# Performance work log

Measured on AMD Instinct MI355X. Metric: run time of the kernel, lower is better.

Reference implementation:

```python
import jax, jax.numpy as jnp
import numpy as np

B, N, H, E, D = 8, 2048, 1024, 8, 2048


def setup_inputs() -> dict:
    key = jax.random.key(0)
    k = jax.random.split(key, 5)
    x = jax.random.normal(k[0], (B, N, H), dtype=jnp.float32)
    Wr = jax.random.normal(k[1], (H, E), dtype=jnp.float32) * 0.02
    br = jnp.zeros((E,), dtype=jnp.float32)
    W1 = jax.random.normal(k[2], (E, H, D), dtype=jnp.float32) * 0.02
    b1 = jnp.zeros((E, D), dtype=jnp.float32)
    W2 = jax.random.normal(k[3], (E, D, H), dtype=jnp.float32) * 0.02
    b2 = jnp.zeros((E, H), dtype=jnp.float32)
    return {"x": x, "Wr": Wr, "br": br, "W1": W1, "b1": b1, "W2": W2, "b2": b2}


def reference(x, Wr, br, W1, b1, W2, b2):
    # x: [B,N,H]; router v1, top-1, eval mode (no expert dropout)
    Bx, Nx, Hx = x.shape
    Ex = Wr.shape[1]
    x_flat = x.reshape(Bx * Nx, Hx)                      # [T,H]
    logits = x_flat @ Wr + br                            # [T,E]
    probs = jax.nn.softmax(logits, axis=-1)              # [T,E]
    expert_idx = jnp.argmax(probs, axis=-1)              # [T]

    out_flat = jnp.zeros_like(x_flat)
    for e in range(Ex):  # small fixed loop over experts
        h = jax.nn.gelu(x_flat @ W1[e] + b1[e], approximate=False)  # exact erf GELU (torch default)
        eout = h @ W2[e] + b2[e]                         # [T,H]
        out_flat = jnp.where((expert_idx == e)[:, None], eout, out_flat)

    out = x + out_flat.reshape(Bx, Nx, Hx)               # residual

    p_i = probs.mean(axis=0)                             # [E]
    balance_loss = Ex * jnp.sum(p_i ** 2)
    EPS = 1e-8
    entropy = -jnp.sum(probs * jnp.log(probs + EPS), axis=-1)
    entropy_loss = entropy.mean()
    tokens_per_expert = jnp.bincount(expert_idx, length=Ex)
    return out, balance_loss, entropy_loss, tokens_per_expert
```

## Files before the change

### kernel.cpp

```cpp
#include <hip/hip_runtime.h>
#include <math.h>

#define TT 16384
#define HH 1024
#define DD 2048
#define EE 8
#define MAXTILES 160

typedef float f32x4 __attribute__((ext_vector_type(4)));
typedef __bf16 bf16x8 __attribute__((ext_vector_type(8)));

__device__ __forceinline__ unsigned short f2bf(float f) {
  union { float f; unsigned u; } v; v.f = f;
  unsigned r = v.u + 0x7FFFu + ((v.u >> 16) & 1u);
  return (unsigned short)(r >> 16);
}

__device__ __forceinline__ void gl2lds16(const unsigned short* g, unsigned short* l) {
  __builtin_amdgcn_global_load_lds(
      (const __attribute__((address_space(1))) void*)g,
      (__attribute__((address_space(3))) void*)l, 16, 0, 0);
}

__global__ void k_init(int* counts, float* probs_sum, float* ent_sum) {
  int t = threadIdx.x;
  if (t < EE) { counts[t] = 0; probs_sum[t] = 0.f; }
  if (t == 0) *ent_sum = 0.f;
}

__global__ __launch_bounds__(256) void k_transpose2(const float* __restrict__ W1s,
                                                    unsigned short* __restrict__ W1d,
                                                    const float* __restrict__ W2s,
                                                    unsigned short* __restrict__ W2d) {
  const int T1 = EE * (HH / 64) * (DD / 64);
  int bid = blockIdx.x;
  const float* src; unsigned short* dst; int R, C;
  if (bid < T1) { src = W1s; dst = W1d; R = HH; C = DD; }
  else          { bid -= T1; src = W2s; dst = W2d; R = DD; C = HH; }
  int tilesC = C >> 6, tilesR = R >> 6;
  int e = bid / (tilesR * tilesC);
  int rem = bid % (tilesR * tilesC);
  int tr = rem / tilesC, tc = rem % tilesC;
  const float* s = src + (size_t)e * R * C + (size_t)(tr * 64) * C + tc * 64;
  unsigned short* d = dst + (size_t)e * R * C + (size_t)(tc * 64) * R + tr * 64;

  __shared__ float t2[64][65];
  int t = threadIdx.x;
  int col = t & 63, rbase = t >> 6;
#pragma unroll
  for (int i = 0; i < 16; ++i) {
    int row = rbase + i * 4;
    t2[col][row] = s[(size_t)row * C + col];
  }
  __syncthreads();
#pragma unroll
  for (int i = 0; i < 4; ++i) {
    int p = t + i * 256;
    int rr = p >> 4, ch = (p & 15) << 2;
    ushort4 o;
    o.x = f2bf(t2[rr][ch + 0]);
    o.y = f2bf(t2[rr][ch + 1]);
    o.z = f2bf(t2[rr][ch + 2]);
    o.w = f2bf(t2[rr][ch + 3]);
    *(ushort4*)&d[(size_t)rr * R + ch] = o;
  }
}

__global__ __launch_bounds__(256) void k_router(const float* __restrict__ x,
                                                const float* __restrict__ Wr,
                                                const float* __restrict__ br,
                                                int* __restrict__ eidx,
                                                float* __restrict__ probs_sum,
                                                float* __restrict__ ent_sum,
                                                int* __restrict__ counts,
                                                unsigned short* __restrict__ xb) {
  __shared__ float s_p[EE];
  __shared__ int   s_c[EE];
  __shared__ float s_e;
  int tid = threadIdx.x;
  if (tid < EE) { s_p[tid] = 0.f; s_c[tid] = 0; }
  if (tid == 0) s_e = 0.f;
  __syncthreads();
  int lane = tid & 63, w = tid >> 6;
  for (int tt = 0; tt < 4; ++tt) {
    int token = blockIdx.x * 16 + w * 4 + tt;
    double acc[EE];
#pragma unroll
    for (int e = 0; e < EE; ++e) acc[e] = 0.0;
    const float* xr = x + (size_t)token * HH;
    unsigned short* xo = xb + (size_t)token * HH;
#pragma unroll
    for (int i = 0; i < 4; ++i) {
      int hh = i * 256 + lane * 4;
      f32x4 xf = *(const f32x4*)&xr[hh];
      ushort4 o;
      o.x = f2bf(xf[0]); o.y = f2bf(xf[1]); o.z = f2bf(xf[2]); o.w = f2bf(xf[3]);
      *(ushort4*)&xo[hh] = o;
#pragma unroll
      for (int k = 0; k < 4; ++k) {
        double xv = (double)xf[k];
        const float* wr = Wr + (size_t)(hh + k) * EE;
#pragma unroll
        for (int e = 0; e < EE; ++e) acc[e] += xv * (double)wr[e];
      }
    }
#pragma unroll
    for (int off = 32; off > 0; off >>= 1) {
#pragma unroll
      for (int e = 0; e < EE; ++e) acc[e] += __shfl_down(acc[e], off);
    }
    if (lane == 0) {
      double l[EE];
#pragma unroll
      for (int e = 0; e < EE; ++e) l[e] = acc[e] + (double)br[e];
      double m = l[0]; int am = 0;
#pragma unroll
      for (int e = 1; e < EE; ++e) { if (l[e] > m) { m = l[e]; am = e; } }
      float p[EE]; float s = 0.f;
#pragma unroll
      for (int e = 0; e < EE; ++e) { p[e] = __expf((float)(l[e] - m)); s += p[e]; }
      float inv = 1.0f / s; float ent = 0.f;
#pragma unroll
      for (int e = 0; e < EE; ++e) { p[e] *= inv; ent -= p[e] * __logf(p[e] + 1e-8f); }
      eidx[token] = am;
#pragma unroll
      for (int e = 0; e < EE; ++e) atomicAdd(&s_p[e], p[e]);
      atomicAdd(&s_e, ent);
      atomicAdd(&s_c[am], 1);
    }
  }
  __syncthreads();
  if (tid < EE) { atomicAdd(&probs_sum[tid], s_p[tid]); atomicAdd(&counts[tid], s_c[tid]); }
  if (tid == 0) atomicAdd(ent_sum, s_e);
}

__global__ __launch_bounds__(256) void k_scan(const int* counts, const float* probs_sum,
                       const float* ent_sum, int* offsets, int* cursor,
                       int* tileE, int* tileR0, int* tileEnd, int* nTiles,
                       float* out_scalars) {
  __shared__ int soff[EE + 1];
  __shared__ int tbase[EE + 1];
  int t = threadIdx.x;
  if (t == 0) {
    int off = 0, tb = 0;
    for (int e = 0; e < EE; ++e) {
      soff[e] = off; offsets[e] = off; cursor[e] = off;
      tbase[e] = tb;
      tb += (counts[e] + 127) >> 7;
      off += counts[e];
    }
    soff[EE] = off; offsets[EE] = off; tbase[EE] = tb;
    *nTiles = tb;
    float bal = 0.f;
    for (int e = 0; e < EE; ++e) { float pi = probs_sum[e] / (float)TT; bal += pi * pi; }
    out_scalars[0] = (float)EE * bal;
    out_scalars[1] = *ent_sum / (float)TT;
    for (int e = 0; e < EE; ++e) out_scalars[2 + e] = (float)counts[e];
  }
  __syncthreads();
  int nt = tbase[EE];
  for (int i = t; i < nt; i += 256) {
    int e = 0;
    while (tbase[e + 1] <= i) ++e;
    int j = i - tbase[e];
    tileE[i] = e; tileR0[i] = soff[e] + j * 128; tileEnd[i] = soff[e] + counts[e];
  }
}

__global__ __launch_bounds__(256) void k_perm(const int* __restrict__ eidx,
                                              int* cursor, int* __restrict__ perm) {
  int t = blockIdx.x * 256 + threadIdx.x;
  int lane = threadIdx.x & 63;
  int mye = eidx[t];
  int pos = 0;
#pragma unroll
  for (int e = 0; e < EE; ++e) {
    unsigned long long mask = __ballot(mye == e);
    if (mask == 0ull) continue;
    int leader = __ffsll(mask) - 1;
    int base = 0;
    if (lane == leader) base = atomicAdd(&cursor[e], __popcll(mask));
    base = __shfl(base, leader);
    if (mye == e) pos = base + (int)__popcll(mask & ((1ull << lane) - 1ull));
  }
  perm[pos] = t;
}


__global__ __launch_bounds__(256) void k_gemm1(const unsigned short* __restrict__ xb,
                                               const unsigned short* __restrict__ Wt1,
                                               const float* __restrict__ b1,
                                               const int* __restrict__ perm,
                                               const int* __restrict__ tileE,
                                               const int* __restrict__ tileR0,
                                               const int* __restrict__ tileEnd,
                                               const int* __restrict__ nTiles,
                                               unsigned short* __restrict__ hbuf) {
  int tile = blockIdx.y;
  if (tile >= *nTiles) return;
  int e = tileE[tile], r0 = tileR0[tile], rend = tileEnd[tile];
  int c0 = blockIdx.x * 128;
  __shared__ __align__(16) unsigned short As[128 * 32];
  __shared__ __align__(16) unsigned short Bs[128 * 32];
  int tid = threadIdx.x, lane = tid & 63, w = tid >> 6;
  int wr = w >> 1, wc = w & 1;
  int quad = lane >> 4, l16 = lane & 15;
  int srow = lane >> 2, seg = lane & 3;
  int ar0 = w * 32 + srow, ar1 = ar0 + 16;
  int g0 = r0 + ar0; if (g0 >= rend) g0 = rend - 1;
  int g1 = r0 + ar1; if (g1 >= rend) g1 = rend - 1;
  const unsigned short* aG0 = xb + (size_t)perm[g0] * HH + seg * 8;
  const unsigned short* aG1 = xb + (size_t)perm[g1] * HH + seg * 8;
  const unsigned short* bBase = Wt1 + (size_t)e * ((size_t)DD * HH);
  const unsigned short* bG0 = bBase + (size_t)(c0 + ar0) * HH + seg * 8;
  const unsigned short* bG1 = bBase + (size_t)(c0 + ar1) * HH + seg * 8;
  unsigned short* aL0 = &As[(w * 32 + 0) * 32];
  unsigned short* aL1 = &As[(w * 32 + 16) * 32];
  unsigned short* bL0 = &Bs[(w * 32 + 0) * 32];
  unsigned short* bL1 = &Bs[(w * 32 + 16) * 32];
  f32x4 acc[4][4] = {};
  for (int k0 = 0; k0 < HH; k0 += 32) {
    gl2lds16(aG0 + k0, aL0);
    gl2lds16(aG1 + k0, aL1);
    gl2lds16(bG0 + k0, bL0);
    gl2lds16(bG1 + k0, bL1);
    __syncthreads();
    bf16x8 a[4], b[4];
#pragma unroll
    for (int i = 0; i < 4; ++i)
      a[i] = *(const bf16x8*)&As[(wr * 64 + i * 16 + l16) * 32 + quad * 8];
#pragma unroll
    for (int j = 0; j < 4; ++j)
      b[j] = *(const bf16x8*)&Bs[(wc * 64 + j * 16 + l16) * 32 + quad * 8];
#pragma unroll
    for (int i = 0; i < 4; ++i)
#pragma unroll
      for (int j = 0; j < 4; ++j)
        acc[i][j] = __builtin_amdgcn_mfma_f32_16x16x32_bf16(a[i], b[j], acc[i][j], 0, 0, 0);
    __syncthreads();
  }
  float bias[4];
#pragma unroll
  for (int j = 0; j < 4; ++j) bias[j] = b1[e * DD + c0 + wc * 64 + j * 16 + l16];
#pragma unroll
  for (int i = 0; i < 4; ++i) {
#pragma unroll
    for (int r = 0; r < 4; ++r) {
      int gr = r0 + wr * 64 + i * 16 + quad * 4 + r;
      if (gr < rend) {
#pragma unroll
        for (int j = 0; j < 4; ++j) {
          int col = c0 + wc * 64 + j * 16 + l16;
          float v = acc[i][j][r] + bias[j];
          v = 0.5f * v * (1.0f + erff(v * 0.70710678118654752f));
          hbuf[(size_t)gr * DD + col] = f2bf(v);
        }
      }
    }
  }
}

__global__ __launch_bounds__(256) void k_gemm2(const unsigned short* __restrict__ hbuf,
                                               const unsigned short* __restrict__ Wt2,
                                               const float* __restrict__ b2,
                                               const float* __restrict__ x,
                                               const int* __restrict__ perm,
                                               const int* __restrict__ tileE,
                                               const int* __restrict__ tileR0,
                                               const int* __restrict__ tileEnd,
                                               const int* __restrict__ nTiles,
                                               float* __restrict__ outp) {
  int tile = blockIdx.y;
  if (tile >= *nTiles) return;
  int e = tileE[tile], r0 = tileR0[tile], rend = tileEnd[tile];
  int c0 = blockIdx.x * 128;
  __shared__ __align__(16) unsigned short As[128 * 32];
  __shared__ __align__(16) unsigned short Bs[128 * 32];
  int tid = threadIdx.x, lane = tid & 63, w = tid >> 6;
  int wr = w >> 1, wc = w & 1;
  int quad = lane >> 4, l16 = lane & 15;
  int srow = lane >> 2, seg = lane & 3;
  int ar0 = w * 32 + srow, ar1 = ar0 + 16;
  int g0 = r0 + ar0; if (g0 >= rend) g0 = rend - 1;
  int g1 = r0 + ar1; if (g1 >= rend) g1 = rend - 1;
  const unsigned short* aG0 = hbuf + (size_t)g0 * DD + seg * 8;
  const unsigned short* aG1 = hbuf + (size_t)g1 * DD + seg * 8;
  const unsigned short* bBase = Wt2 + (size_t)e * ((size_t)HH * DD);
  const unsigned short* bG0 = bBase + (size_t)(c0 + ar0) * DD + seg * 8;
  const unsigned short* bG1 = bBase + (size_t)(c0 + ar1) * DD + seg * 8;
  unsigned short* aL0 = &As[(w * 32 + 0) * 32];
  unsigned short* aL1 = &As[(w * 32 + 16) * 32];
  unsigned short* bL0 = &Bs[(w * 32 + 0) * 32];
  unsigned short* bL1 = &Bs[(w * 32 + 16) * 32];
  f32x4 acc[4][4] = {};
  for (int k0 = 0; k0 < DD; k0 += 32) {
    gl2lds16(aG0 + k0, aL0);
    gl2lds16(aG1 + k0, aL1);
    gl2lds16(bG0 + k0, bL0);
    gl2lds16(bG1 + k0, bL1);
    __syncthreads();
    bf16x8 a[4], b[4];
#pragma unroll
    for (int i = 0; i < 4; ++i)
      a[i] = *(const bf16x8*)&As[(wr * 64 + i * 16 + l16) * 32 + quad * 8];
#pragma unroll
    for (int j = 0; j < 4; ++j)
      b[j] = *(const bf16x8*)&Bs[(wc * 64 + j * 16 + l16) * 32 + quad * 8];
#pragma unroll
    for (int i = 0; i < 4; ++i)
#pragma unroll
      for (int j = 0; j < 4; ++j)
        acc[i][j] = __builtin_amdgcn_mfma_f32_16x16x32_bf16(a[i], b[j], acc[i][j], 0, 0, 0);
    __syncthreads();
  }
  float bias[4];
#pragma unroll
  for (int j = 0; j < 4; ++j) bias[j] = b2[e * HH + c0 + wc * 64 + j * 16 + l16];
#pragma unroll
  for (int i = 0; i < 4; ++i) {
#pragma unroll
    for (int r = 0; r < 4; ++r) {
      int gr = r0 + wr * 64 + i * 16 + quad * 4 + r;
      if (gr < rend) {
        int tok = perm[gr];
#pragma unroll
        for (int j = 0; j < 4; ++j) {
          int col = c0 + wc * 64 + j * 16 + l16;
          size_t oi = (size_t)tok * HH + col;
          outp[oi] = x[oi] + bias[j] + acc[i][j][r];
        }
      }
    }
  }
}

extern "C" void kernel_launch(void* const* d_in, const int* in_sizes, int n_in,
                              void* d_out, int out_size, void* d_ws, size_t ws_size,
                              hipStream_t stream) {
  const float* x  = (const float*)d_in[0];
  const float* Wr = (const float*)d_in[1];
  const float* br = (const float*)d_in[2];
  const float* W1 = (const float*)d_in[3];
  const float* b1 = (const float*)d_in[4];
  const float* W2 = (const float*)d_in[5];
  const float* b2 = (const float*)d_in[6];
  float* outp = (float*)d_out;

  char* ws = (char*)d_ws;
  int*   counts    = (int*)(ws + 0);
  int*   cursor    = (int*)(ws + 64);
  int*   nTiles    = (int*)(ws + 128);
  float* probs_sum = (float*)(ws + 192);
  float* ent_sum   = (float*)(ws + 256);
  int*   offsets   = (int*)(ws + 320);
  int*   tileE     = (int*)(ws + 512);
  int*   tileR0    = (int*)(ws + 2048);
  int*   tileEnd   = (int*)(ws + 3584);
  int*   eidx      = (int*)(ws + 8192);
  int*   perm      = (int*)(ws + 8192 + 4 * (size_t)TT);
  size_t off = 8192 + 8 * (size_t)TT;
  unsigned short* xb   = (unsigned short*)(ws + off); off += (size_t)TT * HH * 2;
  unsigned short* Wt1  = (unsigned short*)(ws + off); off += (size_t)EE * DD * HH * 2;
  unsigned short* Wt2  = (unsigned short*)(ws + off); off += (size_t)EE * HH * DD * 2;
  unsigned short* hbuf = (unsigned short*)(ws + off); off += (size_t)TT * DD * 2;

  k_init<<<1, 64, 0, stream>>>(counts, probs_sum, ent_sum);
  k_transpose2<<<2 * EE * (HH / 64) * (DD / 64), 256, 0, stream>>>(W1, Wt1, W2, Wt2);
  k_router<<<TT / 16, 256, 0, stream>>>(x, Wr, br, eidx, probs_sum, ent_sum, counts, xb);
  k_scan<<<1, 256, 0, stream>>>(counts, probs_sum, ent_sum, offsets, cursor,
                                tileE, tileR0, tileEnd, nTiles, outp + (size_t)TT * HH);
  k_perm<<<TT / 256, 256, 0, stream>>>(eidx, cursor, perm);
  dim3 g1(DD / 128, MAXTILES);
  k_gemm1<<<g1, 256, 0, stream>>>(xb, Wt1, b1, perm, tileE, tileR0, tileEnd, nTiles, hbuf);
  dim3 g2(HH / 128, MAXTILES);
  k_gemm2<<<g2, 256, 0, stream>>>(hbuf, Wt2, b2, x, perm, tileE, tileR0, tileEnd, nTiles, outp);
}
```

Baseline: 574.1 us.

## Deepen GEMM K-tile to 64 with XOR-swizzled LDS and fuse small kernels

```diff
diff --git a/kernel.cpp b/kernel.cpp
--- a/kernel.cpp
+++ b/kernel.cpp
@@ -22,16 +22,17 @@
       (__attribute__((address_space(3))) void*)l, 16, 0, 0);
 }
 
-__global__ void k_init(int* counts, float* probs_sum, float* ent_sum) {
-  int t = threadIdx.x;
-  if (t < EE) { counts[t] = 0; probs_sum[t] = 0.f; }
-  if (t == 0) *ent_sum = 0.f;
-}
-
 __global__ __launch_bounds__(256) void k_transpose2(const float* __restrict__ W1s,
                                                     unsigned short* __restrict__ W1d,
                                                     const float* __restrict__ W2s,
-                                                    unsigned short* __restrict__ W2d) {
+                                                    unsigned short* __restrict__ W2d,
+                                                    int* counts, float* probs_sum,
+                                                    float* ent_sum, int* ticket) {
+  if (blockIdx.x == 0) {
+    int t0 = threadIdx.x;
+    if (t0 < EE) { counts[t0] = 0; probs_sum[t0] = 0.f; }
+    if (t0 == 0) { *ent_sum = 0.f; *ticket = 0; }
+  }
   const int T1 = EE * (HH / 64) * (DD / 64);
   int bid = blockIdx.x;
   const float* src; unsigned short* dst; int R, C;
@@ -73,10 +74,19 @@
                                                 float* __restrict__ probs_sum,
                                                 float* __restrict__ ent_sum,
                                                 int* __restrict__ counts,
-                                                unsigned short* __restrict__ xb) {
+                                                unsigned short* __restrict__ xb,
+                                                int* __restrict__ ticket,
+                                                int* __restrict__ offsets,
+                                                int* __restrict__ cursor,
+                                                int* __restrict__ tileE,
+                                                int* __restrict__ tileR0,
+                                                int* __restrict__ tileEnd,
+                                                int* __restrict__ nTiles,
+                                                float* __restrict__ out_scalars) {
   __shared__ float s_p[EE];
   __shared__ int   s_c[EE];
   __shared__ float s_e;
+  __shared__ int   s_last;
   int tid = threadIdx.x;
   if (tid < EE) { s_p[tid] = 0.f; s_c[tid] = 0; }
   if (tid == 0) s_e = 0.f;
@@ -132,38 +142,41 @@
   __syncthreads();
   if (tid < EE) { atomicAdd(&probs_sum[tid], s_p[tid]); atomicAdd(&counts[tid], s_c[tid]); }
   if (tid == 0) atomicAdd(ent_sum, s_e);
-}
-
-__global__ __launch_bounds__(256) void k_scan(const int* counts, const float* probs_sum,
-                       const float* ent_sum, int* offsets, int* cursor,
-                       int* tileE, int* tileR0, int* tileEnd, int* nTiles,
-                       float* out_scalars) {
-  __shared__ int soff[EE + 1];
-  __shared__ int tbase[EE + 1];
-  int t = threadIdx.x;
-  if (t == 0) {
-    int off = 0, tb = 0;
-    for (int e = 0; e < EE; ++e) {
-      soff[e] = off; offsets[e] = off; cursor[e] = off;
-      tbase[e] = tb;
-      tb += (counts[e] + 127) >> 7;
-      off += counts[e];
-    }
-    soff[EE] = off; offsets[EE] = off; tbase[EE] = tb;
-    *nTiles = tb;
-    float bal = 0.f;
-    for (int e = 0; e < EE; ++e) { float pi = probs_sum[e] / (float)TT; bal += pi * pi; }
-    out_scalars[0] = (float)EE * bal;
-    out_scalars[1] = *ent_sum / (float)TT;
-    for (int e = 0; e < EE; ++e) out_scalars[2 + e] = (float)counts[e];
+  if (tid == 0) {
+    __threadfence();
+    int done = atomicAdd(ticket, 1);
+    s_last = (done == (int)gridDim.x - 1) ? 1 : 0;
   }
   __syncthreads();
-  int nt = tbase[EE];
-  for (int i = t; i < nt; i += 256) {
-    int e = 0;
-    while (tbase[e + 1] <= i) ++e;
-    int j = i - tbase[e];
-    tileE[i] = e; tileR0[i] = soff[e] + j * 128; tileEnd[i] = soff[e] + counts[e];
+  if (s_last) {
+    __shared__ int soff[EE + 1];
+    __shared__ int tbase[EE + 1];
+    __shared__ int scnt[EE];
+    if (tid == 0) {
+      int off = 0, tb = 0; float bal = 0.f;
+      for (int e = 0; e < EE; ++e) {
+        int c = atomicAdd(&counts[e], 0);
+        float ps = atomicAdd(&probs_sum[e], 0.f);
+        scnt[e] = c; soff[e] = off; offsets[e] = off; cursor[e] = off;
+        tbase[e] = tb;
+        tb += (c + 127) >> 7;
+        off += c;
+        float pi = ps / (float)TT; bal += pi * pi;
+        out_scalars[2 + e] = (float)c;
+      }
+      soff[EE] = off; offsets[EE] = off; tbase[EE] = tb;
+      *nTiles = tb;
+      out_scalars[0] = (float)EE * bal;
+      out_scalars[1] = atomicAdd(ent_sum, 0.f) / (float)TT;
+    }
+    __syncthreads();
+    int nt = tbase[EE];
+    for (int i = tid; i < nt; i += 256) {
+      int e = 0;
+      while (tbase[e + 1] <= i) ++e;
+      int j = i - tbase[e];
+      tileE[i] = e; tileR0[i] = soff[e] + j * 128; tileEnd[i] = soff[e] + scnt[e];
+    }
   }
 }
 
@@ -200,43 +213,47 @@
   if (tile >= *nTiles) return;
   int e = tileE[tile], r0 = tileR0[tile], rend = tileEnd[tile];
   int c0 = blockIdx.x * 128;
-  __shared__ __align__(16) unsigned short As[128 * 32];
-  __shared__ __align__(16) unsigned short Bs[128 * 32];
+  __shared__ __align__(16) unsigned short As[128 * 64];
+  __shared__ __align__(16) unsigned short Bs[128 * 64];
   int tid = threadIdx.x, lane = tid & 63, w = tid >> 6;
   int wr = w >> 1, wc = w & 1;
   int quad = lane >> 4, l16 = lane & 15;
-  int srow = lane >> 2, seg = lane & 3;
-  int ar0 = w * 32 + srow, ar1 = ar0 + 16;
-  int g0 = r0 + ar0; if (g0 >= rend) g0 = rend - 1;
-  int g1 = r0 + ar1; if (g1 >= rend) g1 = rend - 1;
-  const unsigned short* aG0 = xb + (size_t)perm[g0] * HH + seg * 8;
-  const unsigned short* aG1 = xb + (size_t)perm[g1] * HH + seg * 8;
+  int lrow = lane >> 3, lslot = lane & 7;
+  int sslot = lslot ^ lrow;
+  const unsigned short* aP[4];
+  const unsigned short* bP[4];
+  unsigned short* aL[4];
+  unsigned short* bL[4];
   const unsigned short* bBase = Wt1 + (size_t)e * ((size_t)DD * HH);
-  const unsigned short* bG0 = bBase + (size_t)(c0 + ar0) * HH + seg * 8;
-  const unsigned short* bG1 = bBase + (size_t)(c0 + ar1) * HH + seg * 8;
-  unsigned short* aL0 = &As[(w * 32 + 0) * 32];
-  unsigned short* aL1 = &As[(w * 32 + 16) * 32];
-  unsigned short* bL0 = &Bs[(w * 32 + 0) * 32];
-  unsigned short* bL1 = &Bs[(w * 32 + 16) * 32];
+#pragma unroll
+  for (int i = 0; i < 4; ++i) {
+    int ar = w * 32 + i * 8 + lrow;
+    int g = r0 + ar; if (g >= rend) g = rend - 1;
+    aP[i] = xb + (size_t)perm[g] * HH + sslot * 8;
+    bP[i] = bBase + (size_t)(c0 + ar) * HH + sslot * 8;
+    aL[i] = &As[(w * 32 + i * 8) * 64];
+    bL[i] = &Bs[(w * 32 + i * 8) * 64];
+  }
   f32x4 acc[4][4] = {};
-  for (int k0 = 0; k0 < HH; k0 += 32) {
-    gl2lds16(aG0 + k0, aL0);
-    gl2lds16(aG1 + k0, aL1);
-    gl2lds16(bG0 + k0, bL0);
-    gl2lds16(bG1 + k0, bL1);
+  for (int k0 = 0; k0 < HH; k0 += 64) {
+#pragma unroll
+    for (int i = 0; i < 4; ++i) { gl2lds16(aP[i] + k0, aL[i]); gl2lds16(bP[i] + k0, bL[i]); }
     __syncthreads();
-    bf16x8 a[4], b[4];
-#pragma unroll
-    for (int i = 0; i < 4; ++i)
-      a[i] = *(const bf16x8*)&As[(wr * 64 + i * 16 + l16) * 32 + quad * 8];
-#pragma unroll
-    for (int j = 0; j < 4; ++j)
-      b[j] = *(const bf16x8*)&Bs[(wc * 64 + j * 16 + l16) * 32 + quad * 8];
-#pragma unroll
-    for (int i = 0; i < 4; ++i)
+#pragma unroll
+    for (int h = 0; h < 2; ++h) {
+      bf16x8 a[4], b[4];
+#pragma unroll
+      for (int i = 0; i < 4; ++i)
+        a[i] = *(const bf16x8*)&As[(wr * 64 + i * 16 + l16) * 64 + (((h << 2) | quad) ^ (l16 & 7)) * 8];
 #pragma unroll
       for (int j = 0; j < 4; ++j)
-        acc[i][j] = __builtin_amdgcn_mfma_f32_16x16x32_bf16(a[i], b[j], acc[i][j], 0, 0, 0);
+        b[j] = *(const bf16x8*)&Bs[(wc * 64 + j * 16 + l16) * 64 + (((h << 2) | quad) ^ (l16 & 7)) * 8];
+#pragma unroll
+      for (int i = 0; i < 4; ++i)
+#pragma unroll
+        for (int j = 0; j < 4; ++j)
+          acc[i][j] = __builtin_amdgcn_mfma_f32_16x16x32_bf16(a[i], b[j], acc[i][j], 0, 0, 0);
+    }
     __syncthreads();
   }
   float bias[4];
@@ -274,43 +291,47 @@
   if (tile >= *nTiles) return;
   int e = tileE[tile], r0 = tileR0[tile], rend = tileEnd[tile];
   int c0 = blockIdx.x * 128;
-  __shared__ __align__(16) unsigned short As[128 * 32];
-  __shared__ __align__(16) unsigned short Bs[128 * 32];
+  __shared__ __align__(16) unsigned short As[128 * 64];
+  __shared__ __align__(16) unsigned short Bs[128 * 64];
   int tid = threadIdx.x, lane = tid & 63, w = tid >> 6;
   int wr = w >> 1, wc = w & 1;
   int quad = lane >> 4, l16 = lane & 15;
-  int srow = lane >> 2, seg = lane & 3;
-  int ar0 = w * 32 + srow, ar1 = ar0 + 16;
-  int g0 = r0 + ar0; if (g0 >= rend) g0 = rend - 1;
-  int g1 = r0 + ar1; if (g1 >= rend) g1 = rend - 1;
-  const unsigned short* aG0 = hbuf + (size_t)g0 * DD + seg * 8;
-  const unsigned short* aG1 = hbuf + (size_t)g1 * DD + seg * 8;
+  int lrow = lane >> 3, lslot = lane & 7;
+  int sslot = lslot ^ lrow;
+  const unsigned short* aP[4];
+  const unsigned short* bP[4];
+  unsigned short* aL[4];
+  unsigned short* bL[4];
   const unsigned short* bBase = Wt2 + (size_t)e * ((size_t)HH * DD);
-  const unsigned short* bG0 = bBase + (size_t)(c0 + ar0) * DD + seg * 8;
-  const unsigned short* bG1 = bBase + (size_t)(c0 + ar1) * DD + seg * 8;
-  unsigned short* aL0 = &As[(w * 32 + 0) * 32];
-  unsigned short* aL1 = &As[(w * 32 + 16) * 32];
-  unsigned short* bL0 = &Bs[(w * 32 + 0) * 32];
-  unsigned short* bL1 = &Bs[(w * 32 + 16) * 32];
+#pragma unroll
+  for (int i = 0; i < 4; ++i) {
+    int ar = w * 32 + i * 8 + lrow;
+    int g = r0 + ar; if (g >= rend) g = rend - 1;
+    aP[i] = hbuf + (size_t)g * DD + sslot * 8;
+    bP[i] = bBase + (size_t)(c0 + ar) * DD + sslot * 8;
+    aL[i] = &As[(w * 32 + i * 8) * 64];
+    bL[i] = &Bs[(w * 32 + i * 8) * 64];
+  }
   f32x4 acc[4][4] = {};
-  for (int k0 = 0; k0 < DD; k0 += 32) {
-    gl2lds16(aG0 + k0, aL0);
-    gl2lds16(aG1 + k0, aL1);
-    gl2lds16(bG0 + k0, bL0);
-    gl2lds16(bG1 + k0, bL1);
+  for (int k0 = 0; k0 < DD; k0 += 64) {
+#pragma unroll
+    for (int i = 0; i < 4; ++i) { gl2lds16(aP[i] + k0, aL[i]); gl2lds16(bP[i] + k0, bL[i]); }
     __syncthreads();
-    bf16x8 a[4], b[4];
-#pragma unroll
-    for (int i = 0; i < 4; ++i)
-      a[i] = *(const bf16x8*)&As[(wr * 64 + i * 16 + l16) * 32 + quad * 8];
-#pragma unroll
-    for (int j = 0; j < 4; ++j)
-      b[j] = *(const bf16x8*)&Bs[(wc * 64 + j * 16 + l16) * 32 + quad * 8];
-#pragma unroll
-    for (int i = 0; i < 4; ++i)
+#pragma unroll
+    for (int h = 0; h < 2; ++h) {
+      bf16x8 a[4], b[4];
+#pragma unroll
+      for (int i = 0; i < 4; ++i)
+        a[i] = *(const bf16x8*)&As[(wr * 64 + i * 16 + l16) * 64 + (((h << 2) | quad) ^ (l16 & 7)) * 8];
 #pragma unroll
       for (int j = 0; j < 4; ++j)
-        acc[i][j] = __builtin_amdgcn_mfma_f32_16x16x32_bf16(a[i], b[j], acc[i][j], 0, 0, 0);
+        b[j] = *(const bf16x8*)&Bs[(wc * 64 + j * 16 + l16) * 64 + (((h << 2) | quad) ^ (l16 & 7)) * 8];
+#pragma unroll
+      for (int i = 0; i < 4; ++i)
+#pragma unroll
+        for (int j = 0; j < 4; ++j)
+          acc[i][j] = __builtin_amdgcn_mfma_f32_16x16x32_bf16(a[i], b[j], acc[i][j], 0, 0, 0);
+    }
     __syncthreads();
   }
   float bias[4];
@@ -353,6 +374,7 @@
   float* probs_sum = (float*)(ws + 192);
   float* ent_sum   = (float*)(ws + 256);
   int*   offsets   = (int*)(ws + 320);
+  int*   ticket    = (int*)(ws + 448);
   int*   tileE     = (int*)(ws + 512);
   int*   tileR0    = (int*)(ws + 2048);
   int*   tileEnd   = (int*)(ws + 3584);
@@ -364,11 +386,13 @@
   unsigned short* Wt2  = (unsigned short*)(ws + off); off += (size_t)EE * HH * DD * 2;
   unsigned short* hbuf = (unsigned short*)(ws + off); off += (size_t)TT * DD * 2;
 
-  k_init<<<1, 64, 0, stream>>>(counts, probs_sum, ent_sum);
-  k_transpose2<<<2 * EE * (HH / 64) * (DD / 64), 256, 0, stream>>>(W1, Wt1, W2, Wt2);
-  k_router<<<TT / 16, 256, 0, stream>>>(x, Wr, br, eidx, probs_sum, ent_sum, counts, xb);
-  k_scan<<<1, 256, 0, stream>>>(counts, probs_sum, ent_sum, offsets, cursor,
-                                tileE, tileR0, tileEnd, nTiles, outp + (size_t)TT * HH);
+  float* out_scalars = outp + (size_t)TT * HH;
+
+  k_transpose2<<<2 * EE * (HH / 64) * (DD / 64), 256, 0, stream>>>(
+      W1, Wt1, W2, Wt2, counts, probs_sum, ent_sum, ticket);
+  k_router<<<TT / 16, 256, 0, stream>>>(x, Wr, br, eidx, probs_sum, ent_sum, counts, xb,
+                                        ticket, offsets, cursor, tileE, tileR0, tileEnd,
+                                        nTiles, out_scalars);
   k_perm<<<TT / 256, 256, 0, stream>>>(eidx, cursor, perm);
   dim3 g1(DD / 128, MAXTILES);
   k_gemm1<<<g1, 256, 0, stream>>>(xb, Wt1, b1, perm, tileE, tileR0, tileEnd, nTiles, hbuf);
```

After: 616.7 us. +7.4%, slower.

## Fuse router, weight transpose and scan into one prep kernel with last-block ticket

Applied to the files above, without the earlier changes.

```diff
diff --git a/kernel.cpp b/kernel.cpp
--- a/kernel.cpp
+++ b/kernel.cpp
@@ -6,6 +6,7 @@
 #define DD 2048
 #define EE 8
 #define MAXTILES 160
+#define RBLK (TT / 16)
 
 typedef float f32x4 __attribute__((ext_vector_type(4)));
 typedef __bf16 bf16x8 __attribute__((ext_vector_type(8)));
@@ -22,148 +23,160 @@
       (__attribute__((address_space(3))) void*)l, 16, 0, 0);
 }
 
-__global__ void k_init(int* counts, float* probs_sum, float* ent_sum) {
+__global__ void k_init(int* counts, float* probs_sum, float* ent_sum, int* ticket) {
   int t = threadIdx.x;
   if (t < EE) { counts[t] = 0; probs_sum[t] = 0.f; }
-  if (t == 0) *ent_sum = 0.f;
-}
-
-__global__ __launch_bounds__(256) void k_transpose2(const float* __restrict__ W1s,
-                                                    unsigned short* __restrict__ W1d,
-                                                    const float* __restrict__ W2s,
-                                                    unsigned short* __restrict__ W2d) {
-  const int T1 = EE * (HH / 64) * (DD / 64);
-  int bid = blockIdx.x;
-  const float* src; unsigned short* dst; int R, C;
-  if (bid < T1) { src = W1s; dst = W1d; R = HH; C = DD; }
-  else          { bid -= T1; src = W2s; dst = W2d; R = DD; C = HH; }
-  int tilesC = C >> 6, tilesR = R >> 6;
-  int e = bid / (tilesR * tilesC);
-  int rem = bid % (tilesR * tilesC);
-  int tr = rem / tilesC, tc = rem % tilesC;
-  const float* s = src + (size_t)e * R * C + (size_t)(tr * 64) * C + tc * 64;
-  unsigned short* d = dst + (size_t)e * R * C + (size_t)(tc * 64) * R + tr * 64;
-
-  __shared__ float t2[64][65];
-  int t = threadIdx.x;
-  int col = t & 63, rbase = t >> 6;
-#pragma unroll
-  for (int i = 0; i < 16; ++i) {
-    int row = rbase + i * 4;
-    t2[col][row] = s[(size_t)row * C + col];
-  }
-  __syncthreads();
-#pragma unroll
-  for (int i = 0; i < 4; ++i) {
-    int p = t + i * 256;
-    int rr = p >> 4, ch = (p & 15) << 2;
-    ushort4 o;
-    o.x = f2bf(t2[rr][ch + 0]);
-    o.y = f2bf(t2[rr][ch + 1]);
-    o.z = f2bf(t2[rr][ch + 2]);
-    o.w = f2bf(t2[rr][ch + 3]);
-    *(ushort4*)&d[(size_t)rr * R + ch] = o;
-  }
-}
-
-__global__ __launch_bounds__(256) void k_router(const float* __restrict__ x,
-                                                const float* __restrict__ Wr,
-                                                const float* __restrict__ br,
-                                                int* __restrict__ eidx,
-                                                float* __restrict__ probs_sum,
-                                                float* __restrict__ ent_sum,
-                                                int* __restrict__ counts,
-                                                unsigned short* __restrict__ xb) {
-  __shared__ float s_p[EE];
-  __shared__ int   s_c[EE];
-  __shared__ float s_e;
+  if (t == 0) { *ent_sum = 0.f; *ticket = 0; }
+}
+
+__global__ __launch_bounds__(256) void k_prep(const float* __restrict__ x,
+                                              const float* __restrict__ Wr,
+                                              const float* __restrict__ br,
+                                              const float* __restrict__ W1s,
+                                              unsigned short* __restrict__ W1d,
+                                              const float* __restrict__ W2s,
+                                              unsigned short* __restrict__ W2d,
+                                              int* __restrict__ eidx,
+                                              float* __restrict__ probs_sum,
+                                              float* __restrict__ ent_sum,
+                                              int* __restrict__ counts,
+                                              unsigned short* __restrict__ xb,
+                                              int* __restrict__ ticket,
+                                              int* __restrict__ offsets,
+                                              int* __restrict__ cursor,
+                                              int* __restrict__ tileE,
+                                              int* __restrict__ tileR0,
+                                              int* __restrict__ tileEnd,
+                                              int* __restrict__ nTiles,
+                                              float* __restrict__ out_scalars) {
+  __shared__ __align__(16) float t2[64][65];
   int tid = threadIdx.x;
-  if (tid < EE) { s_p[tid] = 0.f; s_c[tid] = 0; }
-  if (tid == 0) s_e = 0.f;
-  __syncthreads();
-  int lane = tid & 63, w = tid >> 6;
-  for (int tt = 0; tt < 4; ++tt) {
-    int token = blockIdx.x * 16 + w * 4 + tt;
-    double acc[EE];
-#pragma unroll
-    for (int e = 0; e < EE; ++e) acc[e] = 0.0;
-    const float* xr = x + (size_t)token * HH;
-    unsigned short* xo = xb + (size_t)token * HH;
+
+  if (blockIdx.x < RBLK) {
+    float* s_p   = (float*)&t2[0][0];
+    int*   s_c   = (int*)(s_p + EE);
+    float* s_e   = (float*)(s_c + EE);
+    int*   s_last= (int*)(s_e + 1);
+    if (tid < EE) { s_p[tid] = 0.f; s_c[tid] = 0; }
+    if (tid == 0) *s_e = 0.f;
+    __syncthreads();
+    int lane = tid & 63, w = tid >> 6;
+    for (int tt = 0; tt < 4; ++tt) {
+      int token = blockIdx.x * 16 + w * 4 + tt;
+      double acc[EE];
+#pragma unroll
+      for (int e = 0; e < EE; ++e) acc[e] = 0.0;
+      const float* xr = x + (size_t)token * HH;
+      unsigned short* xo = xb + (size_t)token * HH;
+#pragma unroll
+      for (int i = 0; i < 4; ++i) {
+        int hh = i * 256 + lane * 4;
+        f32x4 xf = *(const f32x4*)&xr[hh];
+        ushort4 o;
+        o.x = f2bf(xf[0]); o.y = f2bf(xf[1]); o.z = f2bf(xf[2]); o.w = f2bf(xf[3]);
+        *(ushort4*)&xo[hh] = o;
+#pragma unroll
+        for (int k = 0; k < 4; ++k) {
+          double xv = (double)xf[k];
+          const float* wr = Wr + (size_t)(hh + k) * EE;
+#pragma unroll
+          for (int e = 0; e < EE; ++e) acc[e] += xv * (double)wr[e];
+        }
+      }
+#pragma unroll
+      for (int off = 32; off > 0; off >>= 1) {
+#pragma unroll
+        for (int e = 0; e < EE; ++e) acc[e] += __shfl_down(acc[e], off);
+      }
+      if (lane == 0) {
+        double l[EE];
+#pragma unroll
+        for (int e = 0; e < EE; ++e) l[e] = acc[e] + (double)br[e];
+        double m = l[0]; int am = 0;
+#pragma unroll
+        for (int e = 1; e < EE; ++e) { if (l[e] > m) { m = l[e]; am = e; } }
+        float p[EE]; float s = 0.f;
+#pragma unroll
+        for (int e = 0; e < EE; ++e) { p[e] = __expf((float)(l[e] - m)); s += p[e]; }
+        float inv = 1.0f / s; float ent = 0.f;
+#pragma unroll
+        for (int e = 0; e < EE; ++e) { p[e] *= inv; ent -= p[e] * __logf(p[e] + 1e-8f); }
+        eidx[token] = am;
+#pragma unroll
+        for (int e = 0; e < EE; ++e) atomicAdd(&s_p[e], p[e]);
+        atomicAdd(s_e, ent);
+        atomicAdd(&s_c[am], 1);
+      }
+    }
+    __syncthreads();
+    if (tid < EE) { atomicAdd(&probs_sum[tid], s_p[tid]); atomicAdd(&counts[tid], s_c[tid]); }
+    if (tid == 0) atomicAdd(ent_sum, *s_e);
+    if (tid == 0) {
+      __threadfence();
+      int done = atomicAdd(ticket, 1);
+      *s_last = (done == RBLK - 1) ? 1 : 0;
+    }
+    __syncthreads();
+    if (*s_last) {
+      int* soff  = (int*)&t2[2][0];
+      int* tbase = soff + (EE + 1);
+      int* scnt  = tbase + (EE + 1);
+      if (tid == 0) {
+        int off = 0, tb = 0; float bal = 0.f;
+        for (int e = 0; e < EE; ++e) {
+          int c = atomicAdd(&counts[e], 0);
+          float ps = atomicAdd(&probs_sum[e], 0.f);
+          scnt[e] = c; soff[e] = off; offsets[e] = off; cursor[e] = off;
+          tbase[e] = tb;
+          tb += (c + 127) >> 7;
+          off += c;
+          float pi = ps / (float)TT; bal += pi * pi;
+          out_scalars[2 + e] = (float)c;
+        }
+        soff[EE] = off; offsets[EE] = off; tbase[EE] = tb;
+        *nTiles = tb;
+        out_scalars[0] = (float)EE * bal;
+        out_scalars[1] = atomicAdd(ent_sum, 0.f) / (float)TT;
+      }
+      __syncthreads();
+      int nt = tbase[EE];
+      for (int i = tid; i < nt; i += 256) {
+        int e = 0;
+        while (tbase[e + 1] <= i) ++e;
+        int j = i - tbase[e];
+        tileE[i] = e; tileR0[i] = soff[e] + j * 128; tileEnd[i] = soff[e] + scnt[e];
+      }
+    }
+  } else {
+    const int T1 = EE * (HH / 64) * (DD / 64);
+    int bid = blockIdx.x - RBLK;
+    const float* src; unsigned short* dst; int R, C;
+    if (bid < T1) { src = W1s; dst = W1d; R = HH; C = DD; }
+    else          { bid -= T1; src = W2s; dst = W2d; R = DD; C = HH; }
+    int tilesC = C >> 6, tilesR = R >> 6;
+    int e = bid / (tilesR * tilesC);
+    int rem = bid % (tilesR * tilesC);
+    int tr = rem / tilesC, tc = rem % tilesC;
+    const float* s = src + (size_t)e * R * C + (size_t)(tr * 64) * C + tc * 64;
+    unsigned short* d = dst + (size_t)e * R * C + (size_t)(tc * 64) * R + tr * 64;
+    int col = tid & 63, rbase = tid >> 6;
+#pragma unroll
+    for (int i = 0; i < 16; ++i) {
+      int row = rbase + i * 4;
+      t2[col][row] = s[(size_t)row * C + col];
+    }
+    __syncthreads();
 #pragma unroll
     for (int i = 0; i < 4; ++i) {
-      int hh = i * 256 + lane * 4;
-      f32x4 xf = *(const f32x4*)&xr[hh];
+      int p = tid + i * 256;
+      int rr = p >> 4, ch = (p & 15) << 2;
       ushort4 o;
-      o.x = f2bf(xf[0]); o.y = f2bf(xf[1]); o.z = f2bf(xf[2]); o.w = f2bf(xf[3]);
-      *(ushort4*)&xo[hh] = o;
-#pragma unroll
-      for (int k = 0; k < 4; ++k) {
-        double xv = (double)xf[k];
-        const float* wr = Wr + (size_t)(hh + k) * EE;
-#pragma unroll
-        for (int e = 0; e < EE; ++e) acc[e] += xv * (double)wr[e];
-      }
-    }
-#pragma unroll
-    for (int off = 32; off > 0; off >>= 1) {
-#pragma unroll
-      for (int e = 0; e < EE; ++e) acc[e] += __shfl_down(acc[e], off);
-    }
-    if (lane == 0) {
-      double l[EE];
-#pragma unroll
-      for (int e = 0; e < EE; ++e) l[e] = acc[e] + (double)br[e];
-      double m = l[0]; int am = 0;
-#pragma unroll
-      for (int e = 1; e < EE; ++e) { if (l[e] > m) { m = l[e]; am = e; } }
-      float p[EE]; float s = 0.f;
-#pragma unroll
-      for (int e = 0; e < EE; ++e) { p[e] = __expf((float)(l[e] - m)); s += p[e]; }
-      float inv = 1.0f / s; float ent = 0.f;
-#pragma unroll
-      for (int e = 0; e < EE; ++e) { p[e] *= inv; ent -= p[e] * __logf(p[e] + 1e-8f); }
-      eidx[token] = am;
-#pragma unroll
-      for (int e = 0; e < EE; ++e) atomicAdd(&s_p[e], p[e]);
-      atomicAdd(&s_e, ent);
-      atomicAdd(&s_c[am], 1);
-    }
-  }
-  __syncthreads();
-  if (tid < EE) { atomicAdd(&probs_sum[tid], s_p[tid]); atomicAdd(&counts[tid], s_c[tid]); }
-  if (tid == 0) atomicAdd(ent_sum, s_e);
-}
-
-__global__ __launch_bounds__(256) void k_scan(const int* counts, const float* probs_sum,
-                       const float* ent_sum, int* offsets, int* cursor,
-                       int* tileE, int* tileR0, int* tileEnd, int* nTiles,
-                       float* out_scalars) {
-  __shared__ int soff[EE + 1];
-  __shared__ int tbase[EE + 1];
-  int t = threadIdx.x;
-  if (t == 0) {
-    int off = 0, tb = 0;
-    for (int e = 0; e < EE; ++e) {
-      soff[e] = off; offsets[e] = off; cursor[e] = off;
-      tbase[e] = tb;
-      tb += (counts[e] + 127) >> 7;
-      off += counts[e];
-    }
-    soff[EE] = off; offsets[EE] = off; tbase[EE] = tb;
-    *nTiles = tb;
-    float bal = 0.f;
-    for (int e = 0; e < EE; ++e) { float pi = probs_sum[e] / (float)TT; bal += pi * pi; }
-    out_scalars[0] = (float)EE * bal;
-    out_scalars[1] = *ent_sum / (float)TT;
-    for (int e = 0; e < EE; ++e) out_scalars[2 + e] = (float)counts[e];
-  }
-  __syncthreads();
-  int nt = tbase[EE];
-  for (int i = t; i < nt; i += 256) {
-    int e = 0;
-    while (tbase[e + 1] <= i) ++e;
-    int j = i - tbase[e];
-    tileE[i] = e; tileR0[i] = soff[e] + j * 128; tileEnd[i] = soff[e] + counts[e];
+      o.x = f2bf(t2[rr][ch + 0]);
+      o.y = f2bf(t2[rr][ch + 1]);
+      o.z = f2bf(t2[rr][ch + 2]);
+      o.w = f2bf(t2[rr][ch + 3]);
+      *(ushort4*)&d[(size_t)rr * R + ch] = o;
+    }
   }
 }
 
@@ -353,6 +366,7 @@
   float* probs_sum = (float*)(ws + 192);
   float* ent_sum   = (float*)(ws + 256);
   int*   offsets   = (int*)(ws + 320);
+  int*   ticket    = (int*)(ws + 448);
   int*   tileE     = (int*)(ws + 512);
   int*   tileR0    = (int*)(ws + 2048);
   int*   tileEnd   = (int*)(ws + 3584);
@@ -364,11 +378,14 @@
   unsigned short* Wt2  = (unsigned short*)(ws + off); off += (size_t)EE * HH * DD * 2;
   unsigned short* hbuf = (unsigned short*)(ws + off); off += (size_t)TT * DD * 2;
 
-  k_init<<<1, 64, 0, stream>>>(counts, probs_sum, ent_sum);
-  k_transpose2<<<2 * EE * (HH / 64) * (DD / 64), 256, 0, stream>>>(W1, Wt1, W2, Wt2);
-  k_router<<<TT / 16, 256, 0, stream>>>(x, Wr, br, eidx, probs_sum, ent_sum, counts, xb);
-  k_scan<<<1, 256, 0, stream>>>(counts, probs_sum, ent_sum, offsets, cursor,
-                                tileE, tileR0, tileEnd, nTiles, outp + (size_t)TT * HH);
+  float* out_scalars = outp + (size_t)TT * HH;
+
+  k_init<<<1, 64, 0, stream>>>(counts, probs_sum, ent_sum, ticket);
+  int prep_grid = RBLK + 2 * EE * (HH / 64) * (DD / 64);
+  k_prep<<<prep_grid, 256, 0, stream>>>(x, Wr, br, W1, Wt1, W2, Wt2,
+                                        eidx, probs_sum, ent_sum, counts, xb,
+                                        ticket, offsets, cursor,
+                                        tileE, tileR0, tileEnd, nTiles, out_scalars);
   k_perm<<<TT / 256, 256, 0, stream>>>(eidx, cursor, perm);
   dim3 g1(DD / 128, MAXTILES);
   k_gemm1<<<g1, 256, 0, stream>>>(xb, Wt1, b1, perm, tileE, tileR0, tileEnd, nTiles, hbuf);
```

Result: slower. 598.1 us (+4.2%).
